# Kernel optimization log

Measured on AMD Instinct MI355X. Metric: run time of the kernel, lower is better.

The kernel has to match this reference:

```python
import jax, jax.numpy as jnp
import numpy as np
import math

B, N, C = 16, 4096, 256
HEADS, HD, SR, FF = 8, 32, 4, 3


def _ln(x, g, b):
    mu = jnp.mean(x, -1, keepdims=True)
    var = jnp.mean((x - mu) ** 2, -1, keepdims=True)
    return (x - mu) / jnp.sqrt(var + 1e-5) * g + b


def _interp(v, out):
    # torch F.interpolate(mode='linear', align_corners=False) along axis 1 of (B,L,C)
    L = v.shape[1]
    c = jnp.clip((jnp.arange(out, dtype=v.dtype) + 0.5) * (L / out) - 0.5, 0.0, L - 1.0)
    i0 = jnp.floor(c).astype(jnp.int32)
    i1 = jnp.minimum(i0 + 1, L - 1)
    w = (c - i0.astype(v.dtype))[None, :, None]
    return v[:, i0] * (1.0 - w) + v[:, i1] * w


def _conv(x, w, b, stride, pad=0, groups=1):
    y = jax.lax.conv_general_dilated(x, w, (stride, stride), ((pad, pad), (pad, pad)),
                                     feature_group_count=groups,
                                     dimension_numbers=('NCHW', 'OIHW', 'NCHW'))
    return y + b[None, :, None, None]


def _lin_attn(q_bhnd, k, v, pe, scale_sp, Wdwc, bdwc, n_kv):
    # NOTE: raw reshape (B,h,N,d)->(B,N,C) as in the torch source (layout quirk kept)
    q = q_bhnd.reshape(B, N, C)
    k = k + pe
    q = jax.nn.relu(q) + 1e-6
    k = jax.nn.relu(k) + 1e-6
    q = q / scale_sp
    k = k / scale_sp
    qn = jnp.linalg.norm(q, axis=-1, keepdims=True)
    kn = jnp.linalg.norm(k, axis=-1, keepdims=True)
    q = q ** FF
    k = k ** FF
    q = q / jnp.linalg.norm(q, axis=-1, keepdims=True) * qn
    k = k / jnp.linalg.norm(k, axis=-1, keepdims=True) * kn
    q = q.reshape(B, N, HEADS, HD).transpose(0, 2, 1, 3)        # (B,h,N,d)
    k = k.reshape(B, n_kv, HEADS, HD).transpose(0, 2, 1, 3)     # (B,h,n,d)
    v = v.reshape(B, n_kv, HEADS, HD).transpose(0, 2, 1, 3)
    km = jnp.mean(k, axis=2)                                     # (B,h,d)
    z = 1.0 / (jnp.einsum('bhnd,bhd->bhn', q, km) + 1e-6)
    s = N ** -0.5
    kv = jnp.einsum('bhnd,bhne->bhde', k * s, v * s)             # (B,h,d,d)
    x = jnp.einsum('bhnd,bhde->bhne', q, kv) * z[..., None]
    v2 = _interp(v.reshape(B, n_kv, C), N)                       # raw reshape quirk kept
    Hs = int(math.isqrt(N))
    x = x.transpose(0, 2, 1, 3).reshape(B, N, C)
    v2 = v2.reshape(B * HEADS, Hs, Hs, HD).transpose(0, 3, 1, 2)  # raw reshape quirk kept
    dv = _conv(v2, Wdwc, bdwc, 1, pad=2, groups=HD).reshape(B, C, N).transpose(0, 2, 1)
    return x + dv


def reference(x, Wq, bq, Wsr1, bsr1, g1, b1, Wsr2, bsr2, g2, b2,
              Wkv1, bkv1, Wkv2, bkv2, pe1, pe2, Wproj, bproj,
              Wdwc, bdwc, scale, H, W):
    q = (x @ Wq.T + bq).reshape(B, N, HEADS, HD).transpose(0, 2, 1, 3)
    x_ = x.transpose(0, 2, 1).reshape(B, C, H, W)
    x1 = jax.nn.gelu(_ln(_conv(x_, Wsr1, bsr1, SR).reshape(B, C, -1).transpose(0, 2, 1), g1, b1), approximate=False)
    x2 = jax.nn.gelu(_ln(_conv(x_, Wsr2, bsr2, SR // 2).reshape(B, C, -1).transpose(0, 2, 1), g2, b2), approximate=False)
    h1, h2 = H // SR, 2 * H // SR
    # 1x1 kv convs as linears; then replicate torch's raw reshape of the NCHW conv output
    y1 = (x1.reshape(B, h1, h1, C) @ Wkv1.T + bkv1).transpose(0, 3, 1, 2).reshape(B, h1, h1, 2 * C).reshape(B, -1, 2, C)
    y2 = (x2.reshape(B, h2, h2, C) @ Wkv2.T + bkv2).transpose(0, 3, 1, 2).reshape(B, h2, h2, 2 * C).reshape(B, -1, 2, C)
    k1, v1 = y1[:, :, 0], y1[:, :, 1]
    k2, v2 = y2[:, :, 0], y2[:, :, 1]
    scale_sp = jax.nn.softplus(scale)
    a1 = _lin_attn(q, k1, v1, pe1, scale_sp, Wdwc, bdwc, N // SR ** 2)
    a2 = _lin_attn(q, k2, v2, pe2, scale_sp, Wdwc, bdwc, 4 * N // SR ** 2)
    return jnp.concatenate([a1, a2], axis=-1) @ Wproj.T + bproj


def setup_inputs() -> dict:
    key = jax.random.key(0)
    ks = jax.random.split(key, 12)
    r = lambda k, s: jax.random.normal(k, s, dtype=jnp.float32) * 0.02
    z = lambda s: jnp.zeros(s, jnp.float32)
    return dict(
        x=jax.random.normal(ks[0], (B, N, C), dtype=jnp.float32),
        Wq=r(ks[1], (C, C)), bq=z((C,)),
        Wsr1=r(ks[2], (C, C, SR, SR)), bsr1=z((C,)),
        g1=jnp.ones((C,), jnp.float32), b1=z((C,)),
        Wsr2=r(ks[3], (C, C, SR // 2, SR // 2)), bsr2=z((C,)),
        g2=jnp.ones((C,), jnp.float32), b2=z((C,)),
        Wkv1=r(ks[4], (2 * C, C)), bkv1=z((2 * C,)),
        Wkv2=r(ks[5], (2 * C, C)), bkv2=z((2 * C,)),
        pe1=r(ks[6], (1, N // (SR * SR), C)),
        pe2=r(ks[7], (1, 4 * N // (SR * SR), C)),
        Wproj=r(ks[8], (C, 2 * C)), bproj=z((C,)),
        Wdwc=r(ks[9], (HD, 1, 5, 5)), bdwc=z((HD,)),
        scale=r(ks[10], (1, 1, C)),
        H=64, W=64,
    )
```

## Files before the change

### kernel.cpp

```cpp
#include <hip/hip_runtime.h>
#include <hip/hip_bf16.h>
#include <cmath>

constexpr int cB = 16;
constexpr int cN = 4096;
constexpr int cC = 256;

typedef __attribute__((ext_vector_type(8))) short short8;
typedef __attribute__((ext_vector_type(4))) float f32x4;

__device__ inline unsigned short bfr(float f) {
  __hip_bfloat16 h = __float2bfloat16(f);
  return *(unsigned short*)&h;
}
__device__ inline float u16tof(unsigned short u) {
  unsigned int v = ((unsigned int)u) << 16;
  return __builtin_bit_cast(float, v);
}

constexpr size_t oWQB    = 0;
constexpr size_t oW1B    = oWQB    + 32768;
constexpr size_t oW2B    = oW1B    + 524288;
constexpr size_t oWKV1B  = oW2B    + 131072;
constexpr size_t oWKV2B  = oWKV1B  + 65536;
constexpr size_t oWPROJB = oWKV2B  + 65536;
constexpr size_t oINVSP  = oWPROJB + 65536;
constexpr size_t oKM1    = oINVSP  + 1024;
constexpr size_t oKV1M   = oKM1    + 4096;
constexpr size_t oKM2    = oKV1M   + 131072;
constexpr size_t oKV2M   = oKM2    + 4096;
constexpr size_t oKVP    = oKV2M   + 131072;
constexpr size_t oKMP    = oKVP    + 524288;
constexpr size_t oQBUF   = oKMP    + 16384;
constexpr size_t oV1G    = oQBUF   + 8388608;
constexpr size_t oV2G    = oV1G    + 524288;
constexpr size_t oU      = oV2G    + 2097152;
constexpr size_t oP1     = oU;
constexpr size_t oX1B    = oU + 4194304;
constexpr size_t oY1     = oU + 4456448;
constexpr size_t oK1P    = oU;
constexpr size_t oX2     = oU;
constexpr size_t oY2     = oU + 4194304;
constexpr size_t oX2B    = oU + 8388608;
constexpr size_t oK2P    = oU;
constexpr size_t oAB     = oU;

__global__ __launch_bounds__(256) void pack_all(
    const float* __restrict__ Wq,   const float* __restrict__ Wkv1,
    const float* __restrict__ Wkv2, const float* __restrict__ Wproj,
    const float* __restrict__ Wsr1, const float* __restrict__ Wsr2,
    const float* __restrict__ scale,
    __hip_bfloat16* WQB, __hip_bfloat16* WKV1B, __hip_bfloat16* WKV2B,
    __hip_bfloat16* WPROJB, __hip_bfloat16* W1B, __hip_bfloat16* W2B,
    float* inv_sp)
{
  int bid = blockIdx.x, tid = threadIdx.x;
  if (bid < 256) {
    int i = bid*256 + tid; WQB[i] = __float2bfloat16(Wq[i]);
  } else if (bid < 768) {
    int i = (bid-256)*256 + tid; WKV1B[i] = __float2bfloat16(Wkv1[i]);
  } else if (bid < 1280) {
    int i = (bid-768)*256 + tid; WKV2B[i] = __float2bfloat16(Wkv2[i]);
  } else if (bid < 1792) {
    int i = (bid-1280)*256 + tid; WPROJB[i] = __float2bfloat16(Wproj[i]);
  } else if (bid < 5888) {
    int i = (bid-1792)*256 + tid;
    int ci = i & 255, rest = i >> 8;
    int p = rest & 15, co = rest >> 4;
    W1B[i] = __float2bfloat16(Wsr1[((size_t)co*256 + ci)*16 + p]);
  } else if (bid < 6912) {
    int i = (bid-5888)*256 + tid;
    int ci = i & 255, rest = i >> 8;
    int p = rest & 3, co = rest >> 2;
    W2B[i] = __float2bfloat16(Wsr2[((size_t)co*256 + ci)*4 + p]);
  } else {
    float v = scale[tid];
    float sp = (v > 20.f) ? v : log1pf(expf(v));
    inv_sp[tid] = 1.f/sp;
  }
}

template<int TM, int TN, int AMODE, int ADT, int EPI>
__global__ __launch_bounds__(256) void gmfma(
    const void* __restrict__ Asrc, const __hip_bfloat16* __restrict__ Bp,
    const float* __restrict__ bias, float* __restrict__ Cout,
    int M, int N, int K, int ldb)
{
  constexpr int APASS = TM/32, BPASS = TN/32;
  constexpr int WGM = (TM==128) ? 2 : ((TN==64) ? 2 : 1);
  constexpr int WGN = 4/WGM;
  constexpr int WM = TM/WGM, WN = TN/WGN;
  constexpr int FM = WM/16, FN = WN/16;
  __shared__ char smem[(TM+TN)*128];
  char* As = smem;
  char* Bs = smem + TM*128;
  const int tid  = threadIdx.x;
  const int row0 = blockIdx.x * TM;
  const int col0 = blockIdx.y * TN;
  const int kbase = blockIdx.z * K;
  const int kq = tid & 7, rl = tid >> 3;
  const int w = tid >> 6, lane = tid & 63;
  const int wr = (WGM==2) ? (w>>1) : 0;
  const int wc = (WGM==2) ? (w&1)  : w;

  f32x4 acc[FM][FN] = {};
  short8 aS[APASS], bS[BPASS];

  auto loadA = [&](int k0) {
    int ka = kbase + k0;
    #pragma unroll
    for (int p = 0; p < APASS; ++p) {
      int r = row0 + rl + p*32;
      const char* ap;
      if (AMODE == 0) {
        if (ADT == 0) ap = (const char*)((const float*)Asrc + (size_t)r*K + k0 + kq*8);
        else          ap = (const char*)((const __hip_bfloat16*)Asrc + (size_t)r*K + k0 + kq*8);
      } else if (AMODE == 1) {
        int b = r >> 8, mm = r & 255;
        int my = mm >> 4, mx = mm & 15;
        int ch = ka >> 8, ky = ch >> 2, kx = ch & 3;
        int tok = (4*my + ky)*64 + 4*mx + kx;
        ap = (const char*)((const float*)Asrc + ((size_t)(b*4096 + tok))*256 + (ka & 255) + kq*8);
      } else {
        int b = r >> 10, mm = r & 1023;
        int my = mm >> 5, mx = mm & 31;
        int ch = ka >> 8, ky = ch >> 1, kx = ch & 1;
        int tok = (2*my + ky)*64 + 2*mx + kx;
        ap = (const char*)((const float*)Asrc + ((size_t)(b*4096 + tok))*256 + (ka & 255) + kq*8);
      }
      if (ADT == 0) {
        float4 v0 = *(const float4*)ap;
        float4 v1 = *(const float4*)(ap + 16);
        short8 s;
        s[0] = (short)bfr(v0.x); s[1] = (short)bfr(v0.y);
        s[2] = (short)bfr(v0.z); s[3] = (short)bfr(v0.w);
        s[4] = (short)bfr(v1.x); s[5] = (short)bfr(v1.y);
        s[6] = (short)bfr(v1.z); s[7] = (short)bfr(v1.w);
        aS[p] = s;
      } else {
        aS[p] = *(const short8*)ap;
      }
    }
  };
  auto loadB = [&](int k0) {
    #pragma unroll
    for (int p = 0; p < BPASS; ++p) {
      int n = col0 + rl + p*32;
      bS[p] = *(const short8*)(Bp + (size_t)n*ldb + kbase + k0 + kq*8);
    }
  };

  loadA(0); loadB(0);
  for (int k0 = 0; k0 < K; k0 += 64) {
    #pragma unroll
    for (int p = 0; p < APASS; ++p) {
      int r = rl + p*32;
      *(short8*)(As + r*128 + ((kq*16) ^ ((r&7)<<4))) = aS[p];
    }
    #pragma unroll
    for (int p = 0; p < BPASS; ++p) {
      int n = rl + p*32;
      *(short8*)(Bs + n*128 + ((kq*16) ^ ((n&7)<<4))) = bS[p];
    }
    __syncthreads();
    if (k0 + 64 < K) { loadA(k0 + 64); loadB(k0 + 64); }
    #pragma unroll
    for (int ks = 0; ks < 2; ++ks) {
      short8 af[FM], bfv[FN];
      #pragma unroll
      for (int i = 0; i < FM; ++i) {
        int r = wr*WM + i*16 + (lane & 15);
        af[i] = *(const short8*)(As + r*128 + ((ks*64 + (lane>>4)*16) ^ ((r&7)<<4)));
      }
      #pragma unroll
      for (int j = 0; j < FN; ++j) {
        int n = wc*WN + j*16 + (lane & 15);
        bfv[j] = *(const short8*)(Bs + n*128 + ((ks*64 + (lane>>4)*16) ^ ((n&7)<<4)));
      }
      #pragma unroll
      for (int i = 0; i < FM; ++i)
        #pragma unroll
        for (int j = 0; j < FN; ++j)
          acc[i][j] = __builtin_amdgcn_mfma_f32_16x16x32_bf16(af[i], bfv[j], acc[i][j], 0, 0, 0);
    }
    __syncthreads();
  }

  #pragma unroll
  for (int i = 0; i < FM; ++i) {
    #pragma unroll
    for (int j = 0; j < FN; ++j) {
      int cc = col0 + wc*WN + j*16 + (lane & 15);
      float bval = (EPI == 2 || EPI == 3) ? 0.f : bias[cc];
      #pragma unroll
      for (int rg = 0; rg < 4; ++rg) {
        int rr = row0 + wr*WM + i*16 + (lane>>4)*4 + rg;
        float v = acc[i][j][rg] + bval;
        if (EPI == 0) {
          Cout[(size_t)rr*N + cc] = v;
        } else if (EPI == 1) {
          int b = rr >> 12, n = rr & 4095;
          int h = cc >> 5, d = cc & 31;
          Cout[((size_t)(b*4096 + h*512 + (n >> 3)))*256 + (n & 7)*32 + d] = v;
        } else if (EPI == 2) {
          Cout[(size_t)rr*N + cc] += v;
        } else if (EPI == 3) {
          Cout[(size_t)blockIdx.z*((size_t)M*N) + (size_t)rr*N + cc] = v;
        } else if (EPI == 4) {
          int b = rr >> 12, n = rr & 4095;
          int h = cc >> 5, d = cc & 31;
          ((__hip_bfloat16*)Cout)[((size_t)(b*4096 + h*512 + (n >> 3)))*256 + (n & 7)*32 + d] =
              __float2bfloat16(v);
        } else {
          ((__hip_bfloat16*)Cout)[(size_t)rr*N + cc] = __float2bfloat16(v);
        }
      }
    }
  }
}

__global__ __launch_bounds__(256) void row_powernorm_bf(__hip_bfloat16* __restrict__ x,
    const float* __restrict__ inv_sp, int rows)
{
  int row = blockIdx.x*4 + (threadIdx.x >> 6);
  if (row >= rows) return;
  int lane = threadIdx.x & 63;
  __hip_bfloat16* p = x + (size_t)row*256 + lane*4;
  ushort4 u = *(ushort4*)p;
  const float4 is = *(const float4*)(inv_sp + lane*4);
  float r0 = (fmaxf(u16tof(u.x),0.f)+1e-6f)*is.x;
  float r1 = (fmaxf(u16tof(u.y),0.f)+1e-6f)*is.y;
  float r2 = (fmaxf(u16tof(u.z),0.f)+1e-6f)*is.z;
  float r3 = (fmaxf(u16tof(u.w),0.f)+1e-6f)*is.w;
  float s2 = r0*r0+r1*r1+r2*r2+r3*r3;
  #pragma unroll
  for (int o = 1; o < 64; o <<= 1) s2 += __shfl_xor(s2, o, 64);
  float c0 = r0*r0*r0, c1 = r1*r1*r1, c2 = r2*r2*r2, c3 = r3*r3*r3;
  float s6 = c0*c0+c1*c1+c2*c2+c3*c3;
  #pragma unroll
  for (int o = 1; o < 64; o <<= 1) s6 += __shfl_xor(s6, o, 64);
  float f = sqrtf(s2/s6);
  ushort4 w;
  w.x = bfr(c0*f); w.y = bfr(c1*f); w.z = bfr(c2*f); w.w = bfr(c3*f);
  *(ushort4*)p = w;
}

__global__ __launch_bounds__(256) void ln_gelu_sum4(const float* __restrict__ P,
    const float* __restrict__ bias, const float* __restrict__ g, const float* __restrict__ bb,
    __hip_bfloat16* __restrict__ outb, int rows)
{
  const size_t PS = (size_t)rows*256;
  int row = blockIdx.x*4 + (threadIdx.x >> 6);
  if (row >= rows) return;
  int lane = threadIdx.x & 63;
  const float* p = P + (size_t)row*256 + lane*4;
  float4 v0 = *(const float4*)p;
  float4 v1 = *(const float4*)(p + PS);
  float4 v2 = *(const float4*)(p + 2*PS);
  float4 v3 = *(const float4*)(p + 3*PS);
  float4 bsv = *(const float4*)(bias + lane*4);
  float4 v;
  v.x = v0.x+v1.x+v2.x+v3.x+bsv.x;
  v.y = v0.y+v1.y+v2.y+v3.y+bsv.y;
  v.z = v0.z+v1.z+v2.z+v3.z+bsv.z;
  v.w = v0.w+v1.w+v2.w+v3.w+bsv.w;
  float s = v.x+v.y+v.z+v.w;
  #pragma unroll
  for (int o = 1; o < 64; o <<= 1) s += __shfl_xor(s, o, 64);
  float mu = s*(1.f/256.f);
  float d0 = v.x-mu, d1 = v.y-mu, d2 = v.z-mu, d3 = v.w-mu;
  float q = d0*d0+d1*d1+d2*d2+d3*d3;
  #pragma unroll
  for (int o = 1; o < 64; o <<= 1) q += __shfl_xor(q, o, 64);
  float rstd = rsqrtf(q*(1.f/256.f) + 1e-5f);
  float4 gv = *(const float4*)(g + lane*4);
  float4 bv = *(const float4*)(bb + lane*4);
  float y0 = d0*rstd*gv.x + bv.x;
  float y1 = d1*rstd*gv.y + bv.y;
  float y2 = d2*rstd*gv.z + bv.z;
  float y3 = d3*rstd*gv.w + bv.w;
  const float k = 0.70710678118654752f;
  ushort4 u;
  u.x = bfr(0.5f*y0*(1.f+erff(y0*k)));
  u.y = bfr(0.5f*y1*(1.f+erff(y1*k)));
  u.z = bfr(0.5f*y2*(1.f+erff(y2*k)));
  u.w = bfr(0.5f*y3*(1.f+erff(y3*k)));
  *(ushort4*)(outb + (size_t)row*256 + lane*4) = u;
}

__global__ __launch_bounds__(256) void ln_gelu_b(const float* __restrict__ x,
    const float* __restrict__ g, const float* __restrict__ bb,
    __hip_bfloat16* __restrict__ outb, int rows)
{
  int row = blockIdx.x*4 + (threadIdx.x >> 6);
  if (row >= rows) return;
  int lane = threadIdx.x & 63;
  const float* p = x + (size_t)row*256 + lane*4;
  float4 v = *(const float4*)p;
  float s = v.x+v.y+v.z+v.w;
  #pragma unroll
  for (int o = 1; o < 64; o <<= 1) s += __shfl_xor(s, o, 64);
  float mu = s*(1.f/256.f);
  float d0 = v.x-mu, d1 = v.y-mu, d2 = v.z-mu, d3 = v.w-mu;
  float q = d0*d0+d1*d1+d2*d2+d3*d3;
  #pragma unroll
  for (int o = 1; o < 64; o <<= 1) q += __shfl_xor(q, o, 64);
  float rstd = rsqrtf(q*(1.f/256.f) + 1e-5f);
  float4 gv = *(const float4*)(g + lane*4);
  float4 bv = *(const float4*)(bb + lane*4);
  float y0 = d0*rstd*gv.x + bv.x;
  float y1 = d1*rstd*gv.y + bv.y;
  float y2 = d2*rstd*gv.z + bv.z;
  float y3 = d3*rstd*gv.w + bv.w;
  const float k = 0.70710678118654752f;
  ushort4 u;
  u.x = bfr(0.5f*y0*(1.f+erff(y0*k)));
  u.y = bfr(0.5f*y1*(1.f+erff(y1*k)));
  u.z = bfr(0.5f*y2*(1.f+erff(y2*k)));
  u.w = bfr(0.5f*y3*(1.f+erff(y3*k)));
  *(ushort4*)(outb + (size_t)row*256 + lane*4) = u;
}

template<int BR>
__global__ __launch_bounds__(256) void gather_kv2(const __hip_bfloat16* __restrict__ y,
    const float* __restrict__ pe, __hip_bfloat16* __restrict__ Ko, __hip_bfloat16* __restrict__ Vo)
{
  constexpr int NKV = (BR == 1) ? 256 : 1024;
  __shared__ float tk[64][65];
  __shared__ float tv[64][65];
  int bid = blockIdx.x;
  int cb = bid & 3;
  int nb = (bid >> 2) % (NKV/64);
  int b  = (bid >> 2) / (NKV/64);
  int n0 = nb*64, c0 = cb*64;
  int tid = threadIdx.x;
  #pragma unroll
  for (int pass = 0; pass < 16; ++pass) {
    int c_l = (tid >> 6)*16 + pass;
    int c = c0 + c_l;
    if (BR == 1) {
      int n_l = tid & 63;
      size_t base = ((size_t)(b*256 + c))*512 + 2*(n0 + n_l);
      tk[c_l][n_l] = __bfloat162float(y[base]);
      tv[c_l][n_l] = __bfloat162float(y[base + 1]);
    } else {
      int u = tid & 31, pp = (tid >> 5) & 1;
      int n_l = 2*u + pp;
      size_t rk = ((size_t)(b*1024 + pp*512 + c))*512 + (size_t)((n0 >> 1) + u);
      tk[c_l][n_l] = __bfloat162float(y[rk]);
      tv[c_l][n_l] = __bfloat162float(y[rk + (size_t)256*512]);
    }
  }
  __syncthreads();
  #pragma unroll
  for (int pass = 0; pass < 16; ++pass) {
    int n_l = (tid >> 6)*16 + pass;
    int c_l = tid & 63;
    int n = n0 + n_l, c = c0 + c_l;
    size_t o = ((size_t)(b*NKV + n))*256 + c;
    Ko[o] = __float2bfloat16(tk[c_l][n_l] + pe[n*256 + c]);
    Vo[o] = __float2bfloat16(tv[c_l][n_l]);
  }
}

__global__ __launch_bounds__(256) void kmkv_part(const __hip_bfloat16* __restrict__ kp,
    const __hip_bfloat16* __restrict__ vg, float* __restrict__ kmp, float* __restrict__ kvp, int nkv)
{
  int g = blockIdx.x;
  int ch = g & 3, bh = g >> 2;
  int b = bh >> 3, h = bh & 7;
  int nchunk = nkv >> 2;
  int tid = threadIdx.x;
  __shared__ float ks[64][32];
  __shared__ float vs[64][32];
  int d  = tid >> 3;
  int e0 = (tid & 7)*4;
  float acc[4] = {0.f,0.f,0.f,0.f};
  float kmacc = 0.f;
  for (int n0 = ch*nchunk; n0 < (ch+1)*nchunk; n0 += 64) {
    #pragma unroll
    for (int i = 0; i < 2; ++i) {
      int f = tid + i*256;
      int nn = f >> 3, q4 = (f & 7)*4;
      size_t base = ((size_t)(b*nkv + n0 + nn))*256 + h*32 + q4;
      ushort4 ku = *(const ushort4*)(kp + base);
      ushort4 vu = *(const ushort4*)(vg + base);
      float4 kf, vf;
      kf.x = u16tof(ku.x); kf.y = u16tof(ku.y); kf.z = u16tof(ku.z); kf.w = u16tof(ku.w);
      vf.x = u16tof(vu.x); vf.y = u16tof(vu.y); vf.z = u16tof(vu.z); vf.w = u16tof(vu.w);
      *(float4*)&ks[nn][q4] = kf;
      *(float4*)&vs[nn][q4] = vf;
    }
    __syncthreads();
    #pragma unroll 8
    for (int nn = 0; nn < 64; ++nn) {
      float kd = ks[nn][d];
      kmacc += kd;
      #pragma unroll
      for (int j = 0; j < 4; ++j) acc[j] += kd * vs[nn][e0+j];
    }
    __syncthreads();
  }
  const float s2c = 1.0f/4096.0f;
  #pragma unroll
  for (int j = 0; j < 4; ++j)
    kvp[(size_t)ch*131072 + ((size_t)bh*32 + e0 + j)*32 + d] = acc[j]*s2c;
  if ((tid & 7) == 0) kmp[ch*4096 + bh*32 + d] = kmacc;
}

__global__ __launch_bounds__(256) void kmkv_red(const float* __restrict__ kmp,
    const float* __restrict__ kvp, float* __restrict__ km, float* __restrict__ kvm, float inv_nkv)
{
  int idx = blockIdx.x*256 + threadIdx.x;
  kvm[idx] = kvp[idx] + kvp[131072 + idx] + kvp[262144 + idx] + kvp[393216 + idx];
  if (idx < 4096)
    km[idx] = (kmp[idx] + kmp[4096 + idx] + kmp[8192 + idx] + kmp[12288 + idx]) * inv_nkv;
}

__global__ __launch_bounds__(512) void attn_mfma(const __hip_bfloat16* __restrict__ q,
    const float* __restrict__ inv_sp,
    const float* __restrict__ km1, const float* __restrict__ kv1,
    const float* __restrict__ km2, const float* __restrict__ kv2,
    __hip_bfloat16* __restrict__ A)
{
  __shared__ __align__(16) char qs[64*512];
  __shared__ __align__(16) char kvs[32*512];
  __shared__ float zsf[2*64*8];
  const int bid = blockIdx.x;
  const int b = bid >> 6, t0 = (bid & 63)*64;
  const int tid = threadIdx.x;

  {
    const float* src = kv1 + (size_t)b*8192;
    for (int i = tid; i < 8192; i += 512) {
      int h = i >> 10, e = (i >> 5) & 31, d = i & 31;
      *(unsigned short*)(kvs + e*512 + ((h*64 + d*2) ^ ((e&7)<<4))) = bfr(src[i]);
    }
  }

  {
    const int h = tid & 7;
    const int t_l = tid >> 3;
    const float* km1p = km1 + b*256 + h*32;
    const float* km2p = km2 + b*256 + h*32;
    const __hip_bfloat16* qp = q + ((size_t)(b*4096 + t0 + t_l))*256 + h*32;
    float cf[32];
    float s2 = 0.f, s6 = 0.f;
    #pragma unroll
    for (int j = 0; j < 4; ++j) {
      short8 qv = *(const short8*)(qp + j*8);
      float4 is0 = *(const float4*)(inv_sp + h*32 + j*8);
      float4 is1 = *(const float4*)(inv_sp + h*32 + j*8 + 4);
      float isv[8] = {is0.x, is0.y, is0.z, is0.w, is1.x, is1.y, is1.z, is1.w};
      #pragma unroll
      for (int k = 0; k < 8; ++k) {
        float val = u16tof((unsigned short)qv[k]);
        float r = (fmaxf(val, 0.f) + 1e-6f) * isv[k];
        s2 += r*r;
        float c = r*r*r;
        s6 += c*c;
        cf[j*8 + k] = c;
      }
    }
    #pragma unroll
    for (int o = 1; o < 8; o <<= 1) {
      s2 += __shfl_xor(s2, o, 64);
      s6 += __shfl_xor(s6, o, 64);
    }
    float f = sqrtf(s2/s6);
    float d1 = 0.f, d2 = 0.f;
    #pragma unroll
    for (int j = 0; j < 8; ++j) {
      float4 k1 = *(const float4*)(km1p + j*4);
      float4 k2 = *(const float4*)(km2p + j*4);
      float q0 = cf[4*j+0]*f, q1 = cf[4*j+1]*f, q2 = cf[4*j+2]*f, q3 = cf[4*j+3]*f;
      cf[4*j+0] = q0; cf[4*j+1] = q1; cf[4*j+2] = q2; cf[4*j+3] = q3;
      d1 += q0*k1.x + q1*k1.y + q2*k1.z + q3*k1.w;
      d2 += q0*k2.x + q1*k2.y + q2*k2.z + q3*k2.w;
    }
    zsf[0*512 + t_l*8 + h] = 1.0f/(d1 + 1e-6f);
    zsf[1*512 + t_l*8 + h] = 1.0f/(d2 + 1e-6f);
    #pragma unroll
    for (int j = 0; j < 4; ++j) {
      short8 s;
      #pragma unroll
      for (int k = 0; k < 8; ++k) s[k] = (short)bfr(cf[j*8+k]);
      *(short8*)(qs + t_l*512 + ((h*64 + j*16) ^ ((t_l&7)<<4))) = s;
    }
  }
  __syncthreads();

  const int h = tid >> 6, l = tid & 63;
  const int lr = l & 15, lk = l >> 4;
  #pragma unroll
  for (int br = 0; br < 2; ++br) {
    if (br == 1) {
      __syncthreads();
      const float* src = kv2 + (size_t)b*8192;
      for (int i = tid; i < 8192; i += 512) {
        int hh = i >> 10, e = (i >> 5) & 31, d = i & 31;
        *(unsigned short*)(kvs + e*512 + ((hh*64 + d*2) ^ ((e&7)<<4))) = bfr(src[i]);
      }
      __syncthreads();
    }
    #pragma unroll
    for (int tt = 0; tt < 4; ++tt) {
      int tr = tt*16 + lr;
      short8 af = *(const short8*)(qs + tr*512 + ((h*64 + lk*16) ^ ((tr&7)<<4)));
      #pragma unroll
      for (int eb = 0; eb < 2; ++eb) {
        int e = eb*16 + lr;
        short8 bf = *(const short8*)(kvs + e*512 + ((h*64 + lk*16) ^ ((e&7)<<4)));
        f32x4 acc = {0.f, 0.f, 0.f, 0.f};
        acc = __builtin_amdgcn_mfma_f32_16x16x32_bf16(af, bf, acc, 0, 0, 0);
        #pragma unroll
        for (int rg = 0; rg < 4; ++rg) {
          int row = lk*4 + rg;
          float z = zsf[br*512 + (tt*16 + row)*8 + h];
          A[((size_t)(b*4096 + t0 + tt*16 + row))*512 + br*256 + h*32 + e] =
              __float2bfloat16(acc[rg]*z);
        }
      }
    }
  }
}

__global__ __launch_bounds__(256) void dwconv_f2m(const __hip_bfloat16* __restrict__ v1,
    const __hip_bfloat16* __restrict__ v2,
    const float* __restrict__ Wd, const float* __restrict__ bias,
    __hip_bfloat16* __restrict__ A)
{
  __shared__ float lds[6*2048];
  int bidx = blockIdx.x;
  bool br2 = bidx >= 4096;
  int wg = br2 ? (bidx - 4096) : bidx;
  const __hip_bfloat16* vg = br2 ? v2 : v1;
  const int broff = br2 ? 256 : 0;
  const int L    = br2 ? 1024 : 256;
  const int RPSH = br2 ? 7 : 5;
  const int NM   = (L >> 3) - 1;
  const float sc = br2 ? 0.25f : 0.0625f;
  const float lmax = (float)(L - 1);

  int wid = (wg & 7)*512 + (wg >> 3);
  int yp = wid & 31;
  int be = wid >> 5;
  int y0 = yp*2;
  int b = be >> 3, e = be & 7;
  int tid = threadIdx.x;

  {
    int d0 = (tid & 7)*4;
    #pragma unroll
    for (int c = 0; c < 2; ++c) {
      int xs = c*32 + (tid >> 3);
      int xg = xs >> 3, xl = xs & 7;
      #pragma unroll
      for (int r = 0; r < 6; ++r) {
        int yy = y0 + r - 2;
        if (yy < 0 || yy > 63) continue;
        int t = e*512 + yy*8 + xg;
        float cpos = ((float)t + 0.5f) * sc - 0.5f;
        cpos = fminf(fmaxf(cpos, 0.0f), lmax);
        int i0 = (int)cpos;
        float w = cpos - (float)i0;
        int i1 = (i0 + 1 < L) ? i0 + 1 : L - 1;
        int n0 = ((i0 & NM) << 3) + xl, ch0 = ((i0 >> RPSH) << 5) + d0;
        int n1 = ((i1 & NM) << 3) + xl, ch1 = ((i1 >> RPSH) << 5) + d0;
        ushort4 au = *(const ushort4*)(vg + ((size_t)(b*L + n0))*256 + ch0);
        ushort4 bu = *(const ushort4*)(vg + ((size_t)(b*L + n1))*256 + ch1);
        float4 o;
        float ax = u16tof(au.x), ay = u16tof(au.y), az = u16tof(au.z), aw = u16tof(au.w);
        o.x = ax + (u16tof(bu.x) - ax)*w;
        o.y = ay + (u16tof(bu.y) - ay)*w;
        o.z = az + (u16tof(bu.z) - az)*w;
        o.w = aw + (u16tof(bu.w) - aw)*w;
        *(float4*)(lds + r*2048 + xs*32 + d0) = o;
      }
    }
  }
  __syncthreads();

  int d = tid & 31, xg = tid >> 5;
  float w[25];
  #pragma unroll
  for (int i = 0; i < 25; ++i) w[i] = Wd[d*25 + i];
  float bv = bias[d];
  #pragma unroll
  for (int rr = 0; rr < 2; ++rr) {
    int y = y0 + rr;
    float acc[8] = {};
    #pragma unroll
    for (int dy = 0; dy < 5; ++dy) {
      int yy = y + dy - 2;
      if (yy >= 0 && yy <= 63) {
        const float* rb = lds + (rr + dy)*2048 + d;
        float in[12];
        #pragma unroll
        for (int i = 0; i < 12; ++i) {
          int xx = xg*8 - 2 + i;
          in[i] = (xx < 0 || xx > 63) ? 0.f : rb[xx*32];
        }
        #pragma unroll
        for (int dx = 0; dx < 5; ++dx) {
          float ww = w[dy*5 + dx];
          #pragma unroll
          for (int j = 0; j < 8; ++j) acc[j] += ww * in[j + dx];
        }
      }
    }
    #pragma unroll
    for (int j = 0; j < 8; ++j) {
      size_t o = ((size_t)(b*4096 + y*64 + xg*8 + j))*512 + broff + e*32 + d;
      float cur = __bfloat162float(A[o]);
      A[o] = __float2bfloat16(cur + acc[j] + bv);
    }
  }
}

extern "C" void kernel_launch(void* const* d_in, const int* in_sizes, int n_in,
                              void* d_out, int out_size, void* d_ws, size_t ws_size,
                              hipStream_t stream)
{
  (void)in_sizes; (void)n_in; (void)out_size; (void)ws_size;
  const float* x     = (const float*)d_in[0];
  const float* Wq    = (const float*)d_in[1];
  const float* bq    = (const float*)d_in[2];
  const float* Wsr1  = (const float*)d_in[3];
  const float* bsr1  = (const float*)d_in[4];
  const float* g1    = (const float*)d_in[5];
  const float* b1    = (const float*)d_in[6];
  const float* Wsr2  = (const float*)d_in[7];
  const float* bsr2  = (const float*)d_in[8];
  const float* g2    = (const float*)d_in[9];
  const float* b2    = (const float*)d_in[10];
  const float* Wkv1  = (const float*)d_in[11];
  const float* bkv1  = (const float*)d_in[12];
  const float* Wkv2  = (const float*)d_in[13];
  const float* bkv2  = (const float*)d_in[14];
  const float* pe1   = (const float*)d_in[15];
  const float* pe2   = (const float*)d_in[16];
  const float* Wproj = (const float*)d_in[17];
  const float* bproj = (const float*)d_in[18];
  const float* Wdwc  = (const float*)d_in[19];
  const float* bdwc  = (const float*)d_in[20];
  const float* scale = (const float*)d_in[21];
  float* out = (float*)d_out;
  float* ws  = (float*)d_ws;
  dim3 blk(256);

  __hip_bfloat16* WQB    = (__hip_bfloat16*)(ws + oWQB);
  __hip_bfloat16* W1B    = (__hip_bfloat16*)(ws + oW1B);
  __hip_bfloat16* W2B    = (__hip_bfloat16*)(ws + oW2B);
  __hip_bfloat16* WKV1B  = (__hip_bfloat16*)(ws + oWKV1B);
  __hip_bfloat16* WKV2B  = (__hip_bfloat16*)(ws + oWKV2B);
  __hip_bfloat16* WPROJB = (__hip_bfloat16*)(ws + oWPROJB);
  __hip_bfloat16* X1B    = (__hip_bfloat16*)(ws + oX1B);
  __hip_bfloat16* X2B    = (__hip_bfloat16*)(ws + oX2B);
  __hip_bfloat16* AB     = (__hip_bfloat16*)(ws + oAB);
  __hip_bfloat16* QB     = (__hip_bfloat16*)(ws + oQBUF);
  __hip_bfloat16* Y1B    = (__hip_bfloat16*)(ws + oY1);
  __hip_bfloat16* Y2B    = (__hip_bfloat16*)(ws + oY2);
  __hip_bfloat16* K1P    = (__hip_bfloat16*)(ws + oK1P);
  __hip_bfloat16* K2P    = (__hip_bfloat16*)(ws + oK2P);
  __hip_bfloat16* V1G    = (__hip_bfloat16*)(ws + oV1G);
  __hip_bfloat16* V2G    = (__hip_bfloat16*)(ws + oV2G);

  pack_all<<<6913, blk, 0, stream>>>(Wq, Wkv1, Wkv2, Wproj, Wsr1, Wsr2, scale,
      WQB, WKV1B, WKV2B, WPROJB, W1B, W2B, ws + oINVSP);

  gmfma<128,128,0,0,4><<<dim3(512,2), blk, 0, stream>>>(x, WQB, bq, (float*)QB, 65536, 256, 256, 256);

  gmfma<64,64,1,0,3><<<dim3(64,4,4), blk, 0, stream>>>(x, W1B, bsr1, ws+oP1, 4096, 256, 1024, 4096);
  ln_gelu_sum4<<<1024, blk, 0, stream>>>(ws+oP1, bsr1, g1, b1, X1B, 4096);
  gmfma<64,64,0,1,5><<<dim3(64,8), blk, 0, stream>>>(X1B, WKV1B, bkv1, (float*)Y1B, 4096, 512, 256, 256);
  gather_kv2<1><<<256, blk, 0, stream>>>(Y1B, pe1, K1P, V1G);
  row_powernorm_bf<<<1024, blk, 0, stream>>>(K1P, ws+oINVSP, 4096);
  kmkv_part<<<512, blk, 0, stream>>>(K1P, V1G, ws+oKMP, ws+oKVP, 256);
  kmkv_red<<<512, blk, 0, stream>>>(ws+oKMP, ws+oKVP, ws+oKM1, ws+oKV1M, 1.0f/256.0f);

  gmfma<64,64,2,0,0><<<dim3(256,4), blk, 0, stream>>>(x, W2B, bsr2, ws+oX2, 16384, 256, 1024, 1024);
  ln_gelu_b<<<4096, blk, 0, stream>>>(ws+oX2, g2, b2, X2B, 16384);
  gmfma<64,64,0,1,5><<<dim3(256,8), blk, 0, stream>>>(X2B, WKV2B, bkv2, (float*)Y2B, 16384, 512, 256, 256);
  gather_kv2<2><<<1024, blk, 0, stream>>>(Y2B, pe2, K2P, V2G);
  row_powernorm_bf<<<4096, blk, 0, stream>>>(K2P, ws+oINVSP, 16384);
  kmkv_part<<<512, blk, 0, stream>>>(K2P, V2G, ws+oKMP, ws+oKVP, 1024);
  kmkv_red<<<512, blk, 0, stream>>>(ws+oKMP, ws+oKVP, ws+oKM2, ws+oKV2M, 1.0f/1024.0f);

  attn_mfma<<<1024, dim3(512), 0, stream>>>(QB, ws+oINVSP,
      ws+oKM1, ws+oKV1M, ws+oKM2, ws+oKV2M, AB);

  dwconv_f2m<<<8192, blk, 0, stream>>>(V1G, V2G, Wdwc, bdwc, AB);

  gmfma<128,128,0,1,0><<<dim3(512,2), blk, 0, stream>>>(AB, WPROJB, bproj, out, 65536, 256, 512, 512);
}
```

Before: 314.6 us.

## Merge branch-1 and branch-2 KV post-processing kernels into combined launches

The gather, power-norm, partial kv/km and reduction kernels for the two spatial-reduction branches are merged so each runs once over both branches, dispatching on block index. Branch-1 intermediates (X1B, Y1, K1P) and the partial buffers get their own workspace regions so they survive while branch 2 is computed. This cuts four kernel launches and lets the small branch-1 grids share the GPU with branch 2, at the cost of more workspace memory and some runtime branching inside the kernels.

```diff
diff --git a/kernel.cpp b/kernel.cpp
--- a/kernel.cpp
+++ b/kernel.cpp
@@ -29,16 +29,18 @@
 constexpr size_t oKV1M   = oKM1    + 4096;
 constexpr size_t oKM2    = oKV1M   + 131072;
 constexpr size_t oKV2M   = oKM2    + 4096;
-constexpr size_t oKVP    = oKV2M   + 131072;
-constexpr size_t oKMP    = oKVP    + 524288;
-constexpr size_t oQBUF   = oKMP    + 16384;
+constexpr size_t oKVP1   = oKV2M   + 131072;
+constexpr size_t oKMP1   = oKVP1   + 524288;
+constexpr size_t oKVP2   = oKMP1   + 16384;
+constexpr size_t oKMP2   = oKVP2   + 524288;
+constexpr size_t oQBUF   = oKMP2   + 16384;
 constexpr size_t oV1G    = oQBUF   + 8388608;
 constexpr size_t oV2G    = oV1G    + 524288;
-constexpr size_t oU      = oV2G    + 2097152;
+constexpr size_t oX1B    = oV2G    + 2097152;
+constexpr size_t oY1     = oX1B    + 262144;
+constexpr size_t oK1P    = oY1     + 1048576;
+constexpr size_t oU      = oK1P    + 524288;
 constexpr size_t oP1     = oU;
-constexpr size_t oX1B    = oU + 4194304;
-constexpr size_t oY1     = oU + 4456448;
-constexpr size_t oK1P    = oU;
 constexpr size_t oX2     = oU;
 constexpr size_t oY2     = oU + 4194304;
 constexpr size_t oX2B    = oU + 8388608;
@@ -219,13 +221,13 @@
   }
 }
 
-__global__ __launch_bounds__(256) void row_powernorm_bf(__hip_bfloat16* __restrict__ x,
-    const float* __restrict__ inv_sp, int rows)
+__global__ __launch_bounds__(256) void row_powernorm_m(__hip_bfloat16* __restrict__ k1,
+    __hip_bfloat16* __restrict__ k2, const float* __restrict__ inv_sp)
 {
   int row = blockIdx.x*4 + (threadIdx.x >> 6);
-  if (row >= rows) return;
   int lane = threadIdx.x & 63;
-  __hip_bfloat16* p = x + (size_t)row*256 + lane*4;
+  __hip_bfloat16* p = (row < 4096) ? (k1 + (size_t)row*256 + lane*4)
+                                   : (k2 + (size_t)(row-4096)*256 + lane*4);
   ushort4 u = *(ushort4*)p;
   const float4 is = *(const float4*)(inv_sp + lane*4);
   float r0 = (fmaxf(u16tof(u.x),0.f)+1e-6f)*is.x;
@@ -321,14 +323,23 @@
   *(ushort4*)(outb + (size_t)row*256 + lane*4) = u;
 }
 
-template<int BR>
-__global__ __launch_bounds__(256) void gather_kv2(const __hip_bfloat16* __restrict__ y,
-    const float* __restrict__ pe, __hip_bfloat16* __restrict__ Ko, __hip_bfloat16* __restrict__ Vo)
-{
-  constexpr int NKV = (BR == 1) ? 256 : 1024;
+__global__ __launch_bounds__(256) void gather_m(const __hip_bfloat16* __restrict__ y1,
+    const __hip_bfloat16* __restrict__ y2,
+    const float* __restrict__ pe1, const float* __restrict__ pe2,
+    __hip_bfloat16* __restrict__ K1, __hip_bfloat16* __restrict__ V1,
+    __hip_bfloat16* __restrict__ K2, __hip_bfloat16* __restrict__ V2)
+{
   __shared__ float tk[64][65];
   __shared__ float tv[64][65];
-  int bid = blockIdx.x;
+  int bidx = blockIdx.x;
+  bool br2 = bidx >= 256;
+  int bid = br2 ? (bidx - 256) : bidx;
+  const __hip_bfloat16* y = br2 ? y2 : y1;
+  const float* pe = br2 ? pe2 : pe1;
+  __hip_bfloat16* Ko = br2 ? K2 : K1;
+  __hip_bfloat16* Vo = br2 ? V2 : V1;
+  const int NKV = br2 ? 1024 : 256;
+
   int cb = bid & 3;
   int nb = (bid >> 2) % (NKV/64);
   int b  = (bid >> 2) / (NKV/64);
@@ -338,7 +349,7 @@
   for (int pass = 0; pass < 16; ++pass) {
     int c_l = (tid >> 6)*16 + pass;
     int c = c0 + c_l;
-    if (BR == 1) {
+    if (!br2) {
       int n_l = tid & 63;
       size_t base = ((size_t)(b*256 + c))*512 + 2*(n0 + n_l);
       tk[c_l][n_l] = __bfloat162float(y[base]);
@@ -363,10 +374,21 @@
   }
 }
 
-__global__ __launch_bounds__(256) void kmkv_part(const __hip_bfloat16* __restrict__ kp,
-    const __hip_bfloat16* __restrict__ vg, float* __restrict__ kmp, float* __restrict__ kvp, int nkv)
+__global__ __launch_bounds__(256) void kmkv_part_m(const __hip_bfloat16* __restrict__ k1,
+    const __hip_bfloat16* __restrict__ v1, const __hip_bfloat16* __restrict__ k2,
+    const __hip_bfloat16* __restrict__ v2,
+    float* __restrict__ kmp1, float* __restrict__ kvp1,
+    float* __restrict__ kmp2, float* __restrict__ kvp2)
 {
   int g = blockIdx.x;
+  bool br2 = g >= 512;
+  if (br2) g -= 512;
+  const __hip_bfloat16* kp = br2 ? k2 : k1;
+  const __hip_bfloat16* vg = br2 ? v2 : v1;
+  float* kmp = br2 ? kmp2 : kmp1;
+  float* kvp = br2 ? kvp2 : kvp1;
+  const int nkv = br2 ? 1024 : 256;
+
   int ch = g & 3, bh = g >> 2;
   int b = bh >> 3, h = bh & 7;
   int nchunk = nkv >> 2;
@@ -408,10 +430,20 @@
   if ((tid & 7) == 0) kmp[ch*4096 + bh*32 + d] = kmacc;
 }
 
-__global__ __launch_bounds__(256) void kmkv_red(const float* __restrict__ kmp,
-    const float* __restrict__ kvp, float* __restrict__ km, float* __restrict__ kvm, float inv_nkv)
+__global__ __launch_bounds__(256) void kmkv_red_m(const float* __restrict__ kmp1,
+    const float* __restrict__ kvp1, const float* __restrict__ kmp2,
+    const float* __restrict__ kvp2,
+    float* __restrict__ km1, float* __restrict__ kvm1,
+    float* __restrict__ km2, float* __restrict__ kvm2)
 {
   int idx = blockIdx.x*256 + threadIdx.x;
+  bool br2 = idx >= 131072;
+  if (br2) idx -= 131072;
+  const float* kmp = br2 ? kmp2 : kmp1;
+  const float* kvp = br2 ? kvp2 : kvp1;
+  float* km = br2 ? km2 : km1;
+  float* kvm = br2 ? kvm2 : kvm1;
+  float inv_nkv = br2 ? (1.0f/1024.0f) : (1.0f/256.0f);
   kvm[idx] = kvp[idx] + kvp[131072 + idx] + kvp[262144 + idx] + kvp[393216 + idx];
   if (idx < 4096)
     km[idx] = (kmp[idx] + kmp[4096 + idx] + kmp[8192 + idx] + kmp[12288 + idx]) * inv_nkv;
@@ -674,18 +706,16 @@
   gmfma<64,64,1,0,3><<<dim3(64,4,4), blk, 0, stream>>>(x, W1B, bsr1, ws+oP1, 4096, 256, 1024, 4096);
   ln_gelu_sum4<<<1024, blk, 0, stream>>>(ws+oP1, bsr1, g1, b1, X1B, 4096);
   gmfma<64,64,0,1,5><<<dim3(64,8), blk, 0, stream>>>(X1B, WKV1B, bkv1, (float*)Y1B, 4096, 512, 256, 256);
-  gather_kv2<1><<<256, blk, 0, stream>>>(Y1B, pe1, K1P, V1G);
-  row_powernorm_bf<<<1024, blk, 0, stream>>>(K1P, ws+oINVSP, 4096);
-  kmkv_part<<<512, blk, 0, stream>>>(K1P, V1G, ws+oKMP, ws+oKVP, 256);
-  kmkv_red<<<512, blk, 0, stream>>>(ws+oKMP, ws+oKVP, ws+oKM1, ws+oKV1M, 1.0f/256.0f);
-
   gmfma<64,64,2,0,0><<<dim3(256,4), blk, 0, stream>>>(x, W2B, bsr2, ws+oX2, 16384, 256, 1024, 1024);
   ln_gelu_b<<<4096, blk, 0, stream>>>(ws+oX2, g2, b2, X2B, 16384);
   gmfma<64,64,0,1,5><<<dim3(256,8), blk, 0, stream>>>(X2B, WKV2B, bkv2, (float*)Y2B, 16384, 512, 256, 256);
-  gather_kv2<2><<<1024, blk, 0, stream>>>(Y2B, pe2, K2P, V2G);
-  row_powernorm_bf<<<4096, blk, 0, stream>>>(K2P, ws+oINVSP, 16384);
-  kmkv_part<<<512, blk, 0, stream>>>(K2P, V2G, ws+oKMP, ws+oKVP, 1024);
-  kmkv_red<<<512, blk, 0, stream>>>(ws+oKMP, ws+oKVP, ws+oKM2, ws+oKV2M, 1.0f/1024.0f);
+
+  gather_m<<<1280, blk, 0, stream>>>(Y1B, Y2B, pe1, pe2, K1P, V1G, K2P, V2G);
+  row_powernorm_m<<<5120, blk, 0, stream>>>(K1P, K2P, ws+oINVSP);
+  kmkv_part_m<<<1024, blk, 0, stream>>>(K1P, V1G, K2P, V2G,
+      ws+oKMP1, ws+oKVP1, ws+oKMP2, ws+oKVP2);
+  kmkv_red_m<<<1024, blk, 0, stream>>>(ws+oKMP1, ws+oKVP1, ws+oKMP2, ws+oKVP2,
+      ws+oKM1, ws+oKV1M, ws+oKM2, ws+oKV2M);
 
   attn_mfma<<<1024, dim3(512), 0, stream>>>(QB, ws+oINVSP,
       ws+oKM1, ws+oKV1M, ws+oKM2, ws+oKV2M, AB);
```

Result: no change. 311.6 us (median of 2 runs) (-0.9%).
